# Optimization experiments

Measured on AMD Instinct MI355X. Metric: run time of the kernel, lower is better.

The kernel has to match this reference:

```python
import jax, jax.numpy as jnp
import numpy as np

N_EMBD = 1024
N_HEAD = 16

def setup_inputs() -> dict:
    key = jax.random.key(0)
    ks = jax.random.split(key, 5)
    s = 0.02
    x = jax.random.normal(ks[0], (4, 2048, N_EMBD), dtype=jnp.float32)
    W_attn = jax.random.normal(ks[1], (N_EMBD, 3 * N_EMBD), dtype=jnp.float32) * s
    b_attn = jnp.zeros((3 * N_EMBD,), dtype=jnp.float32)
    W_proj = jax.random.normal(ks[2], (N_EMBD, N_EMBD), dtype=jnp.float32) * s
    b_proj = jnp.zeros((N_EMBD,), dtype=jnp.float32)
    return {"x": x, "W_attn": W_attn, "b_attn": b_attn, "W_proj": W_proj, "b_proj": b_proj}

def reference(x, W_attn, b_attn, W_proj, b_proj):
    B, T, C = x.shape
    H = N_HEAD
    Dh = C // H
    qkv = x @ W_attn + b_attn                      # [B,T,3C]
    q, k, v = jnp.split(qkv, 3, axis=2)
    # [B,T,C] -> [B,H,T,Dh]
    q = q.reshape(B, T, H, Dh).transpose(0, 2, 1, 3)
    k = k.reshape(B, T, H, Dh).transpose(0, 2, 1, 3)
    v = v.reshape(B, T, H, Dh).transpose(0, 2, 1, 3)
    scale = 1.0 / jnp.sqrt(jnp.asarray(Dh, dtype=x.dtype))
    att = jnp.einsum('bhqd,bhkd->bhqk', q, k) * scale   # [B,H,T,T]
    causal = jnp.tril(jnp.ones((T, T), dtype=bool))
    att = jnp.where(causal[None, None], att, jnp.asarray(-jnp.inf, dtype=att.dtype))
    att = jax.nn.softmax(att, axis=-1)
    out = jnp.einsum('bhqk,bhkd->bhqd', att, v)          # [B,H,T,Dh]
    out = out.transpose(0, 2, 1, 3).reshape(B, T, C)
    return out @ W_proj + b_proj
```

## Files before the change

kernel.cpp:

```cpp
#include <hip/hip_runtime.h>
#include <hip/hip_bf16.h>
#include <cstdint>

typedef unsigned short u16;
typedef __attribute__((ext_vector_type(8))) short bf16x8;
typedef __attribute__((ext_vector_type(4))) float f32x4;

#define AS1 __attribute__((address_space(1)))
#define AS3 __attribute__((address_space(3)))

#define QSCALE_CONST 0.18033688011112042f
#define SMAX_CONST 8.0f

__device__ __forceinline__ u16 f2bf(float f) {
  union { float f; unsigned u; } v; v.f = f;
  unsigned u = v.u;
  return (u16)((u + 0x7fffu + ((u >> 16) & 1u)) >> 16);
}

__device__ __forceinline__ void gload_lds16(const void* g, const void* l) {
  __builtin_amdgcn_global_load_lds(
      (const AS1 unsigned int*)(uintptr_t)g,
      (AS3 unsigned int*)(unsigned int)(uintptr_t)l,
      16, 0, 0);
}

__global__ __launch_bounds__(256) void cast_bf16_kernel(
    const float* __restrict__ in, u16* __restrict__ out, int n) {
  int i = (blockIdx.x * 256 + threadIdx.x) * 4;
  if (i >= n) return;
  float4 f = *(const float4*)(in + i);
  ushort4 o;
  o.x = f2bf(f.x); o.y = f2bf(f.y); o.z = f2bf(f.z); o.w = f2bf(f.w);
  *(ushort4*)(out + i) = o;
}

__global__ __launch_bounds__(256) void transpose_cast_kernel(
    const float* __restrict__ in, u16* __restrict__ outT, int R, int C) {
  __shared__ float tile[32][33];
  const int c0 = blockIdx.x << 5, r0 = blockIdx.y << 5;
  const int x = threadIdx.x & 31, y = threadIdx.x >> 5;
#pragma unroll
  for (int yy = y; yy < 32; yy += 8)
    tile[yy][x] = in[(size_t)(r0 + yy) * C + c0 + x];
  __syncthreads();
#pragma unroll
  for (int yy = y; yy < 32; yy += 8)
    outT[(size_t)(c0 + yy) * R + r0 + x] = f2bf(tile[x][yy]);
}

template <typename OutT>
__global__ __launch_bounds__(256, 3) void gemm_bf16_kernel(
    const u16* __restrict__ A, const u16* __restrict__ Bt,
    const float* __restrict__ bias, OutT* __restrict__ Cmat,
    int M, int N, int K, int qcols) {
  __shared__ __attribute__((aligned(16))) u16 As[3][128 * 32];
  __shared__ __attribute__((aligned(16))) u16 Bs[3][128 * 32];

  const int nbn = N >> 7;
  const int nwg = (M >> 7) * nbn;
  int bid = blockIdx.x;
  if ((nwg & 7) == 0) {
    int cpx = nwg >> 3;
    bid = (bid & 7) * cpx + (bid >> 3);
  }
  const int bm = bid / nbn, bn = bid % nbn;

  const int tid = threadIdx.x;
  const int lane = tid & 63, wave = tid >> 6;
  const int g = lane >> 4, l15 = lane & 15;
  const int wrow = (wave >> 1) << 6, wcol = (wave & 1) << 6;

  const u16* Abase = A + (size_t)(bm << 7) * K;
  const u16* Bbase = Bt + (size_t)(bn << 7) * K;

  const int c0_ = wave * 64 + lane, c1_ = 256 + c0_;
  const int row0_ = c0_ >> 2, row1_ = c1_ >> 2;
  const size_t soff0 = (size_t)row0_ * K + ((c0_ & 3) ^ (row0_ & 3)) * 8;
  const size_t soff1 = (size_t)row1_ * K + ((c1_ & 3) ^ (row1_ & 3)) * 8;
  const int doff0 = c0_ * 8, doff1 = c1_ * 8;

  auto stage = [&](int buf, int k0) {
    gload_lds16(Abase + k0 + soff0, As[buf] + doff0);
    gload_lds16(Bbase + k0 + soff0, Bs[buf] + doff0);
    gload_lds16(Abase + k0 + soff1, As[buf] + doff1);
    gload_lds16(Bbase + k0 + soff1, Bs[buf] + doff1);
  };

  f32x4 zero = {0.f, 0.f, 0.f, 0.f};
  f32x4 acc[4][4];
#pragma unroll
  for (int i = 0; i < 4; ++i)
#pragma unroll
    for (int j = 0; j < 4; ++j) acc[i][j] = zero;

  const int NT = K >> 5;
  stage(0, 0);
  stage(1, 32);
#pragma unroll 1
  for (int kt = 0; kt < NT; ++kt) {
    const int cur = kt % 3;
    asm volatile("s_waitcnt lgkmcnt(0)" ::: "memory");
    __builtin_amdgcn_sched_barrier(0);
    if (kt < NT - 1) asm volatile("s_waitcnt vmcnt(4)" ::: "memory");
    else             asm volatile("s_waitcnt vmcnt(0)" ::: "memory");
    __builtin_amdgcn_s_barrier();
    if (kt + 2 < NT) stage((kt + 2) % 3, (kt + 2) << 5);

    const char* Ab = (const char*)As[cur];
    const char* Bb = (const char*)Bs[cur];
    bf16x8 af[4], bfr[4];
#pragma unroll
    for (int i = 0; i < 4; ++i) {
      int ra = wrow + i * 16 + l15;
      af[i] = *(const bf16x8*)(Ab + ra * 64 + ((g * 16) ^ ((ra & 3) << 4)));
      int rb = wcol + i * 16 + l15;
      bfr[i] = *(const bf16x8*)(Bb + rb * 64 + ((g * 16) ^ ((rb & 3) << 4)));
    }
#pragma unroll
    for (int i = 0; i < 4; ++i)
#pragma unroll
      for (int j = 0; j < 4; ++j)
        acc[i][j] = __builtin_amdgcn_mfma_f32_16x16x32_bf16(af[i], bfr[j], acc[i][j], 0, 0, 0);
  }

#pragma unroll
  for (int i = 0; i < 4; ++i) {
    int row0 = (bm << 7) + wrow + i * 16 + g * 4;
#pragma unroll
    for (int j = 0; j < 4; ++j) {
      int col = (bn << 7) + wcol + j * 16 + l15;
      float bv = bias[col];
      const bool qc = col < qcols;
#pragma unroll
      for (int r = 0; r < 4; ++r) {
        float v = acc[i][j][r] + bv;
        if (qc) v *= QSCALE_CONST;
        size_t idx = (size_t)(row0 + r) * N + col;
        if constexpr (sizeof(OutT) == 2)
          ((u16*)Cmat)[idx] = f2bf(v);
        else
          ((float*)Cmat)[idx] = v;
      }
    }
  }
}

__global__ __launch_bounds__(256, 2) void attn_kernel(
    const u16* __restrict__ qkv, u16* __restrict__ aout) {
  __shared__ __attribute__((aligned(16))) char KsB[2][8192];
  __shared__ __attribute__((aligned(16))) char VtB[2][8192];
  __shared__ __attribute__((aligned(16))) char PbB[4][4096];

  const int bh = blockIdx.x;
  const int b = bh >> 4, h = bh & 15;
  const int tid = threadIdx.x, lane = tid & 63, wave = tid >> 6;
  const int g = lane >> 4, l15 = lane & 15;

  const u16* qbase = qkv + (size_t)b * 2048 * 3072 + h * 64;
  const u16* kbase = qbase + 1024;
  const u16* vbase = qbase + 2048;

  const int krow0 = tid >> 3;
  const int ksc = (tid & 7) ^ (krow0 & 7);
  const size_t ksrc0 = (size_t)krow0 * 3072 + ksc * 8;
  const size_t ksrc1 = ksrc0 + (size_t)32 * 3072;
  const int vp_ = tid >> 3, vdh = tid & 7;
  const size_t vsrc = (size_t)(2 * vp_) * 3072 + vdh * 8;
  const int vkc = vp_ >> 2, vofs = (vp_ & 3) << 2;

  char* pb = PbB[wave];
  const f32x4 sinit = {-SMAX_CONST, -SMAX_CONST, -SMAX_CONST, -SMAX_CONST};
  f32x4 zero = {0.f, 0.f, 0.f, 0.f};

#pragma unroll 1
  for (int jj = 0; jj < 2; ++jj) {
    const int j = jj ? (15 - blockIdx.y) : blockIdx.y;
    const int q0 = j << 7;
    const int qrow = q0 + wave * 32;
    const int nt = 2 * j + 2;

    bf16x8 qfA[2], qfB[2];
#pragma unroll
    for (int kf = 0; kf < 2; ++kf) {
      qfA[kf] = *(const bf16x8*)(qbase + (size_t)(qrow + l15) * 3072 + kf * 32 + g * 8);
      qfB[kf] = *(const bf16x8*)(qbase + (size_t)(qrow + 16 + l15) * 3072 + kf * 32 + g * 8);
    }

    float lsumA = 0.f, lsumB = 0.f;
    f32x4 oA[4], oB[4];
#pragma unroll
    for (int d = 0; d < 4; ++d) { oA[d] = zero; oB[d] = zero; }

    gload_lds16(kbase + ksrc0, KsB[0] + wave * 1024);
    gload_lds16(kbase + ksrc1, KsB[0] + 4096 + wave * 1024);
    {
      bf16x8 v0 = *(const bf16x8*)(vbase + vsrc);
      bf16x8 v1 = *(const bf16x8*)(vbase + vsrc + 3072);
      char* vb = VtB[0];
#pragma unroll
      for (int q = 0; q < 8; ++q) {
        int d = vdh * 8 + q;
        int sig = q ^ vdh;
        unsigned pack = (unsigned)(u16)v0[q] | ((unsigned)(u16)v1[q] << 16);
        *(unsigned*)(vb + d * 128 + ((vkc ^ sig) << 4) + vofs) = pack;
      }
    }

    bf16x8 nv0, nv1;
#pragma unroll 1
    for (int t = 0; t < nt; ++t) {
      const int cur = t & 1;
      const int kv0 = t << 6;
      const bool pre = (t + 1 < nt);
      __syncthreads();

      if (pre) {
        const size_t nxt = (size_t)(t + 1) * 196608;
        gload_lds16(kbase + nxt + ksrc0, KsB[cur ^ 1] + wave * 1024);
        gload_lds16(kbase + nxt + ksrc1, KsB[cur ^ 1] + 4096 + wave * 1024);
        nv0 = *(const bf16x8*)(vbase + nxt + vsrc);
        nv1 = *(const bf16x8*)(vbase + nxt + vsrc + 3072);
      }

      if (qrow + 31 >= kv0) {
        const char* ks = KsB[cur];
        f32x4 sA[4], sB[4];
#pragma unroll
        for (int n = 0; n < 4; ++n) { sA[n] = sinit; sB[n] = sinit; }
#pragma unroll
        for (int kf = 0; kf < 2; ++kf)
#pragma unroll
          for (int n = 0; n < 4; ++n) {
            int row = n * 16 + l15;
            bf16x8 kfr = *(const bf16x8*)(ks + row * 128 + (((kf * 4 + g) ^ (row & 7)) << 4));
            sA[n] = __builtin_amdgcn_mfma_f32_16x16x32_bf16(kfr, qfA[kf], sA[n], 0, 0, 0);
            sB[n] = __builtin_amdgcn_mfma_f32_16x16x32_bf16(kfr, qfB[kf], sB[n], 0, 0, 0);
          }

        const int kvb = kv0 + g * 4;
        if (kv0 + 63 > qrow) {
          const int qgA = qrow + l15;
#pragma unroll
          for (int n = 0; n < 4; ++n)
#pragma unroll
            for (int r = 0; r < 4; ++r)
              if (kvb + n * 16 + r > qgA) sA[n][r] = -1e30f;
        }
        if (kv0 + 63 > qrow + 16) {
          const int qgB = qrow + 16 + l15;
#pragma unroll
          for (int n = 0; n < 4; ++n)
#pragma unroll
            for (int r = 0; r < 4; ++r)
              if (kvb + n * 16 + r > qgB) sB[n][r] = -1e30f;
        }

        float rsA = 0.f, rsB = 0.f;
#pragma unroll
        for (int n = 0; n < 4; ++n)
#pragma unroll
          for (int r = 0; r < 4; ++r) {
            float pA = __builtin_amdgcn_exp2f(sA[n][r]);
            float pB = __builtin_amdgcn_exp2f(sB[n][r]);
            sA[n][r] = pA; rsA += pA;
            sB[n][r] = pB; rsB += pB;
          }
        lsumA += rsA; lsumB += rsB;

#pragma unroll
        for (int n = 0; n < 4; ++n) {
          uint2 wA, wB;
          asm("v_cvt_pk_bf16_f32 %0, %1, %2" : "=v"(wA.x) : "v"(sA[n][0]), "v"(sA[n][1]));
          asm("v_cvt_pk_bf16_f32 %0, %1, %2" : "=v"(wA.y) : "v"(sA[n][2]), "v"(sA[n][3]));
          asm("v_cvt_pk_bf16_f32 %0, %1, %2" : "=v"(wB.x) : "v"(sB[n][0]), "v"(sB[n][1]));
          asm("v_cvt_pk_bf16_f32 %0, %1, %2" : "=v"(wB.y) : "v"(sB[n][2]), "v"(sB[n][3]));
          int c = n * 2 + (g >> 1);
          int boff = (((c ^ (l15 & 7)) << 4) | ((g & 1) << 3)) + l15 * 128;
          *(uint2*)(pb + boff) = wA;
          *(uint2*)(pb + 2048 + boff) = wB;
        }

        const char* vt = VtB[cur];
        bf16x8 pfA[2], pfB[2];
#pragma unroll
        for (int kf = 0; kf < 2; ++kf) {
          int poff = l15 * 128 + (((kf * 4 + g) ^ (l15 & 7)) << 4);
          pfA[kf] = *(const bf16x8*)(pb + poff);
          pfB[kf] = *(const bf16x8*)(pb + 2048 + poff);
        }
#pragma unroll
        for (int kf = 0; kf < 2; ++kf)
#pragma unroll
          for (int d = 0; d < 4; ++d) {
            int dr = d * 16 + l15;
            int sig = (dr & 7) ^ ((dr >> 3) & 7);
            bf16x8 vf = *(const bf16x8*)(vt + dr * 128 + (((kf * 4 + g) ^ sig) << 4));
            oA[d] = __builtin_amdgcn_mfma_f32_16x16x32_bf16(pfA[kf], vf, oA[d], 0, 0, 0);
            oB[d] = __builtin_amdgcn_mfma_f32_16x16x32_bf16(pfB[kf], vf, oB[d], 0, 0, 0);
          }
      }

      if (pre) {
        char* vb = VtB[cur ^ 1];
#pragma unroll
        for (int q = 0; q < 8; ++q) {
          int d = vdh * 8 + q;
          int sig = q ^ vdh;
          unsigned pack = (unsigned)(u16)nv0[q] | ((unsigned)(u16)nv1[q] << 16);
          *(unsigned*)(vb + d * 128 + ((vkc ^ sig) << 4) + vofs) = pack;
        }
      }
    }

    lsumA += __shfl_xor(lsumA, 16); lsumA += __shfl_xor(lsumA, 32);
    lsumB += __shfl_xor(lsumB, 16); lsumB += __shfl_xor(lsumB, 32);
    float invA[4], invB[4];
#pragma unroll
    for (int r = 0; r < 4; ++r) {
      invA[r] = __builtin_amdgcn_rcpf(__shfl(lsumA, g * 4 + r));
      invB[r] = __builtin_amdgcn_rcpf(__shfl(lsumB, g * 4 + r));
    }
    const size_t obase = (size_t)(b * 2048 + qrow) * 1024 + h * 64;
#pragma unroll
    for (int d = 0; d < 4; ++d)
#pragma unroll
      for (int r = 0; r < 4; ++r) {
        aout[obase + (size_t)(g * 4 + r) * 1024 + d * 16 + l15] = f2bf(oA[d][r] * invA[r]);
        aout[obase + (size_t)(16 + g * 4 + r) * 1024 + d * 16 + l15] = f2bf(oB[d][r] * invB[r]);
      }
  }
}

extern "C" void kernel_launch(void* const* d_in, const int* in_sizes, int n_in,
                              void* d_out, int out_size, void* d_ws, size_t ws_size,
                              hipStream_t stream) {
  const float* x      = (const float*)d_in[0];
  const float* W_attn = (const float*)d_in[1];
  const float* b_attn = (const float*)d_in[2];
  const float* W_proj = (const float*)d_in[3];
  const float* b_proj = (const float*)d_in[4];
  float* out = (float*)d_out;

  char* ws = (char*)d_ws;
  u16* xb   = (u16*)(ws);
  u16* Wat  = (u16*)(ws + (size_t)16 * 1024 * 1024);
  u16* Wpt  = (u16*)(ws + (size_t)22 * 1024 * 1024);
  u16* qkv  = (u16*)(ws + (size_t)24 * 1024 * 1024);
  u16* aout = (u16*)(ws + (size_t)72 * 1024 * 1024);

  cast_bf16_kernel<<<8192, 256, 0, stream>>>(x, xb, 8388608);
  transpose_cast_kernel<<<dim3(96, 32), 256, 0, stream>>>(W_attn, Wat, 1024, 3072);
  transpose_cast_kernel<<<dim3(32, 32), 256, 0, stream>>>(W_proj, Wpt, 1024, 1024);
  gemm_bf16_kernel<u16><<<1536, 256, 0, stream>>>(xb, Wat, b_attn, qkv, 8192, 3072, 1024, 1024);
  attn_kernel<<<dim3(64, 8), 256, 0, stream>>>(qkv, aout);
  gemm_bf16_kernel<float><<<512, 256, 0, stream>>>(aout, Wpt, b_proj, out, 8192, 1024, 1024, 0);
}
```

Measured before the change: 166.7 us.

## Use 256x256-tile 8-wave GEMM kernel for QKV projection

Adds a new bf16 GEMM kernel with 256x256 output tiles, 512 threads (8 waves, each computing 128x64), triple-buffered LDS staging and a split two-phase MFMA schedule that interleaves the A and B loads with compute. It replaces the 128x128 GEMM for the QKV projection, cutting the launch to 384 workgroups. Larger tiles raise arithmetic intensity and reduce global/L2 traffic per FLOP. In exchange, register pressure and LDS use per workgroup go up, and fewer workgroups means worse load balance across the CUs.

```diff
diff --git a/kernel.cpp b/kernel.cpp
--- a/kernel.cpp
+++ b/kernel.cpp
@@ -47,6 +47,131 @@
 #pragma unroll
   for (int yy = y; yy < 32; yy += 8)
     outT[(size_t)(c0 + yy) * R + r0 + x] = f2bf(tile[x][yy]);
+}
+
+__global__ __launch_bounds__(512, 2) void gemm256_kernel(
+    const u16* __restrict__ A, const u16* __restrict__ Bt,
+    const float* __restrict__ bias, u16* __restrict__ Cmat,
+    int M, int N, int K, int qcols) {
+  __shared__ __attribute__((aligned(16))) u16 As[3][256 * 32];
+  __shared__ __attribute__((aligned(16))) u16 Bs[3][256 * 32];
+
+  const int nbn = N >> 8;
+  const int nwg = (M >> 8) * nbn;
+  int bid = blockIdx.x;
+  if ((nwg & 7) == 0) {
+    int cpx = nwg >> 3;
+    bid = (bid & 7) * cpx + (bid >> 3);
+  }
+  const int bm = bid / nbn, bn = bid % nbn;
+
+  const int tid = threadIdx.x;
+  const int lane = tid & 63, wave = tid >> 6;
+  const int g = lane >> 4, l15 = lane & 15;
+  const int wm = wave >> 2, wn = wave & 3;
+
+  const u16* Abase = A + (size_t)(bm << 8) * K;
+  const u16* Bbase = Bt + (size_t)(bn << 8) * K;
+
+  const int c0_ = tid, c1_ = 512 + tid;
+  const int r0_ = c0_ >> 2, r1_ = c1_ >> 2;
+  const size_t soff0 = (size_t)r0_ * K + ((c0_ & 3) ^ (r0_ & 3)) * 8;
+  const size_t soff1 = (size_t)r1_ * K + ((c1_ & 3) ^ (r1_ & 3)) * 8;
+  const int doff0 = c0_ * 8, doff1 = c1_ * 8;
+
+  auto stageA = [&](int buf, int k0) {
+    gload_lds16(Abase + k0 + soff0, As[buf] + doff0);
+    gload_lds16(Abase + k0 + soff1, As[buf] + doff1);
+  };
+  auto stageB = [&](int buf, int k0) {
+    gload_lds16(Bbase + k0 + soff0, Bs[buf] + doff0);
+    gload_lds16(Bbase + k0 + soff1, Bs[buf] + doff1);
+  };
+
+  f32x4 zero = {0.f, 0.f, 0.f, 0.f};
+  f32x4 acc[8][4];
+#pragma unroll
+  for (int i = 0; i < 8; ++i)
+#pragma unroll
+    for (int j = 0; j < 4; ++j) acc[i][j] = zero;
+
+  const int NT = K >> 5;
+  stageA(0, 0); stageB(0, 0);
+  stageA(1, 32); stageB(1, 32);
+  asm volatile("s_waitcnt vmcnt(4)" ::: "memory");
+  __builtin_amdgcn_s_barrier();
+  __builtin_amdgcn_sched_barrier(0);
+
+#pragma unroll 1
+  for (int kt = 0; kt < NT; ++kt) {
+    const int cur = kt % 3, nxt = (kt + 2) % 3;
+    const char* Ab = (const char*)As[cur];
+    const char* Bb = (const char*)Bs[cur];
+
+    bf16x8 af[4], bfr[4];
+#pragma unroll
+    for (int i = 0; i < 4; ++i) {
+      int ra = wm * 128 + i * 16 + l15;
+      af[i] = *(const bf16x8*)(Ab + ra * 64 + ((g ^ (ra & 3)) << 4));
+    }
+#pragma unroll
+    for (int j = 0; j < 4; ++j) {
+      int rb = wn * 64 + j * 16 + l15;
+      bfr[j] = *(const bf16x8*)(Bb + rb * 64 + ((g ^ (rb & 3)) << 4));
+    }
+    if (kt + 2 < NT) stageA(nxt, (kt + 2) << 5);
+    __builtin_amdgcn_s_barrier();
+    asm volatile("s_waitcnt lgkmcnt(0)" ::: "memory");
+    __builtin_amdgcn_sched_barrier(0);
+    __builtin_amdgcn_s_setprio(1);
+#pragma unroll
+    for (int i = 0; i < 4; ++i)
+#pragma unroll
+      for (int j = 0; j < 4; ++j)
+        acc[i][j] = __builtin_amdgcn_mfma_f32_16x16x32_bf16(af[i], bfr[j], acc[i][j], 0, 0, 0);
+    __builtin_amdgcn_s_setprio(0);
+    __builtin_amdgcn_s_barrier();
+    __builtin_amdgcn_sched_barrier(0);
+
+    bf16x8 ag[4];
+#pragma unroll
+    for (int i = 0; i < 4; ++i) {
+      int ra = wm * 128 + (i + 4) * 16 + l15;
+      ag[i] = *(const bf16x8*)(Ab + ra * 64 + ((g ^ (ra & 3)) << 4));
+    }
+    if (kt + 2 < NT) stageB(nxt, (kt + 2) << 5);
+    __builtin_amdgcn_s_barrier();
+    asm volatile("s_waitcnt lgkmcnt(0)" ::: "memory");
+    __builtin_amdgcn_sched_barrier(0);
+    __builtin_amdgcn_s_setprio(1);
+#pragma unroll
+    for (int i = 0; i < 4; ++i)
+#pragma unroll
+      for (int j = 0; j < 4; ++j)
+        acc[i + 4][j] = __builtin_amdgcn_mfma_f32_16x16x32_bf16(ag[i], bfr[j], acc[i + 4][j], 0, 0, 0);
+    __builtin_amdgcn_s_setprio(0);
+    if (kt < NT - 2)       asm volatile("s_waitcnt vmcnt(4)" ::: "memory");
+    else if (kt == NT - 2) asm volatile("s_waitcnt vmcnt(0)" ::: "memory");
+    __builtin_amdgcn_s_barrier();
+    __builtin_amdgcn_sched_barrier(0);
+  }
+
+#pragma unroll
+  for (int i = 0; i < 8; ++i) {
+    int row0 = (bm << 8) + wm * 128 + i * 16 + g * 4;
+#pragma unroll
+    for (int j = 0; j < 4; ++j) {
+      int col = (bn << 8) + wn * 64 + j * 16 + l15;
+      float bv = bias[col];
+      const bool qc = col < qcols;
+#pragma unroll
+      for (int r = 0; r < 4; ++r) {
+        float v = acc[i][j][r] + bv;
+        if (qc) v *= QSCALE_CONST;
+        Cmat[(size_t)(row0 + r) * N + col] = f2bf(v);
+      }
+    }
+  }
 }
 
 template <typename OutT>
@@ -352,7 +477,7 @@
   cast_bf16_kernel<<<8192, 256, 0, stream>>>(x, xb, 8388608);
   transpose_cast_kernel<<<dim3(96, 32), 256, 0, stream>>>(W_attn, Wat, 1024, 3072);
   transpose_cast_kernel<<<dim3(32, 32), 256, 0, stream>>>(W_proj, Wpt, 1024, 1024);
-  gemm_bf16_kernel<u16><<<1536, 256, 0, stream>>>(xb, Wat, b_attn, qkv, 8192, 3072, 1024, 1024);
+  gemm256_kernel<<<384, 512, 0, stream>>>(xb, Wat, b_attn, qkv, 8192, 3072, 1024, 1024);
   attn_kernel<<<dim3(64, 8), 256, 0, stream>>>(qkv, aout);
   gemm_bf16_kernel<float><<<512, 256, 0, stream>>>(aout, Wpt, b_proj, out, 8192, 1024, 1024, 0);
 }
```

After: 170.5 us. 1.02x slower.

## Enlarge GEMM tiles to 128x256 with 8 waves and double-buffered 64-wide K stages

Applied to the files above, without the earlier changes.

Rewrites the bf16 GEMM to use 512-thread workgroups computing 128x256 output tiles, with K stepped in 64-wide chunks split into two 32-wide LDS sub-stages that are double-buffered. The next tile's global-to-LDS loads are issued between the fragment reads and the MFMAs, and the MFMA block is wrapped in s_setprio, to overlap memory with compute and improve operand reuse per LDS load. The LDS swizzle changes to an (row>>1)-based XOR. This trades more LDS per workgroup and fewer resident workgroups, plus fewer blocks for the second GEMM (256), for larger tiles and fewer barriers per K.

```diff
diff --git a/kernel.cpp b/kernel.cpp
--- a/kernel.cpp
+++ b/kernel.cpp
@@ -50,14 +50,14 @@
 }
 
 template <typename OutT>
-__global__ __launch_bounds__(256, 3) void gemm_bf16_kernel(
+__global__ __launch_bounds__(512, 2) void gemm1_kernel(
     const u16* __restrict__ A, const u16* __restrict__ Bt,
     const float* __restrict__ bias, OutT* __restrict__ Cmat,
     int M, int N, int K, int qcols) {
-  __shared__ __attribute__((aligned(16))) u16 As[3][128 * 32];
-  __shared__ __attribute__((aligned(16))) u16 Bs[3][128 * 32];
-
-  const int nbn = N >> 7;
+  __shared__ __attribute__((aligned(16))) u16 LA[2][2][128 * 32];
+  __shared__ __attribute__((aligned(16))) u16 LB[2][2][256 * 32];
+
+  const int nbn = N >> 8;
   const int nwg = (M >> 7) * nbn;
   int bid = blockIdx.x;
   if ((nwg & 7) == 0) {
@@ -69,22 +69,23 @@
   const int tid = threadIdx.x;
   const int lane = tid & 63, wave = tid >> 6;
   const int g = lane >> 4, l15 = lane & 15;
-  const int wrow = (wave >> 1) << 6, wcol = (wave & 1) << 6;
+  const int wm = wave >> 2, wn = wave & 3;
 
   const u16* Abase = A + (size_t)(bm << 7) * K;
-  const u16* Bbase = Bt + (size_t)(bn << 7) * K;
-
-  const int c0_ = wave * 64 + lane, c1_ = 256 + c0_;
-  const int row0_ = c0_ >> 2, row1_ = c1_ >> 2;
-  const size_t soff0 = (size_t)row0_ * K + ((c0_ & 3) ^ (row0_ & 3)) * 8;
-  const size_t soff1 = (size_t)row1_ * K + ((c1_ & 3) ^ (row1_ & 3)) * 8;
-  const int doff0 = c0_ * 8, doff1 = c1_ * 8;
-
-  auto stage = [&](int buf, int k0) {
-    gload_lds16(Abase + k0 + soff0, As[buf] + doff0);
-    gload_lds16(Bbase + k0 + soff0, Bs[buf] + doff0);
-    gload_lds16(Abase + k0 + soff1, As[buf] + doff1);
-    gload_lds16(Bbase + k0 + soff1, Bs[buf] + doff1);
+  const u16* Bbase = Bt + (size_t)(bn << 8) * K;
+
+  const int rA = tid >> 2;
+  const size_t aoff = (size_t)rA * K + (((tid & 3) ^ ((rA >> 1) & 3)) * 8);
+  const int rB0 = tid >> 2;
+  const size_t boff0 = (size_t)rB0 * K + (((tid & 3) ^ ((rB0 >> 1) & 3)) * 8);
+  const int cB1 = 512 + tid, rB1 = cB1 >> 2;
+  const size_t boff1 = (size_t)rB1 * K + (((cB1 & 3) ^ ((rB1 >> 1) & 3)) * 8);
+
+  auto stageG = [&](int buf, int s, int kt) {
+    const size_t kof = (size_t)kt * 64 + s * 32;
+    gload_lds16(Abase + kof + aoff, &LA[buf][s][0] + tid * 8);
+    gload_lds16(Bbase + kof + boff0, &LB[buf][s][0] + tid * 8);
+    gload_lds16(Bbase + kof + boff1, &LB[buf][s][0] + (512 + tid) * 8);
   };
 
   f32x4 zero = {0.f, 0.f, 0.f, 0.f};
@@ -94,42 +95,56 @@
 #pragma unroll
     for (int j = 0; j < 4; ++j) acc[i][j] = zero;
 
-  const int NT = K >> 5;
-  stage(0, 0);
-  stage(1, 32);
+  const int NT = K >> 6;
+
+  stageG(0, 0, 0);
+  stageG(0, 1, 0);
+  asm volatile("s_waitcnt vmcnt(3)" ::: "memory");
+  __builtin_amdgcn_s_barrier();
+  __builtin_amdgcn_sched_barrier(0);
+
 #pragma unroll 1
   for (int kt = 0; kt < NT; ++kt) {
-    const int cur = kt % 3;
-    asm volatile("s_waitcnt lgkmcnt(0)" ::: "memory");
-    __builtin_amdgcn_sched_barrier(0);
-    if (kt < NT - 1) asm volatile("s_waitcnt vmcnt(4)" ::: "memory");
-    else             asm volatile("s_waitcnt vmcnt(0)" ::: "memory");
-    __builtin_amdgcn_s_barrier();
-    if (kt + 2 < NT) stage((kt + 2) % 3, (kt + 2) << 5);
-
-    const char* Ab = (const char*)As[cur];
-    const char* Bb = (const char*)Bs[cur];
-    bf16x8 af[4], bfr[4];
-#pragma unroll
-    for (int i = 0; i < 4; ++i) {
-      int ra = wrow + i * 16 + l15;
-      af[i] = *(const bf16x8*)(Ab + ra * 64 + ((g * 16) ^ ((ra & 3) << 4)));
-      int rb = wcol + i * 16 + l15;
-      bfr[i] = *(const bf16x8*)(Bb + rb * 64 + ((g * 16) ^ ((rb & 3) << 4)));
-    }
-#pragma unroll
-    for (int i = 0; i < 4; ++i)
-#pragma unroll
-      for (int j = 0; j < 4; ++j)
-        acc[i][j] = __builtin_amdgcn_mfma_f32_16x16x32_bf16(af[i], bfr[j], acc[i][j], 0, 0, 0);
+    const int cbuf = kt & 1, nbuf = cbuf ^ 1;
+    const bool more = (kt + 1 < NT);
+#pragma unroll
+    for (int s = 0; s < 2; ++s) {
+      const char* Ab = (const char*)&LA[cbuf][s][0];
+      const char* Bb = (const char*)&LB[cbuf][s][0];
+      bf16x8 af[4], bfr[4];
+#pragma unroll
+      for (int i = 0; i < 4; ++i) {
+        int ra = wm * 64 + i * 16 + l15;
+        af[i] = *(const bf16x8*)(Ab + ra * 64 + ((g ^ ((ra >> 1) & 3)) << 4));
+      }
+#pragma unroll
+      for (int j = 0; j < 4; ++j) {
+        int rb = wn * 64 + j * 16 + l15;
+        bfr[j] = *(const bf16x8*)(Bb + rb * 64 + ((g ^ ((rb >> 1) & 3)) << 4));
+      }
+      if (more) stageG(nbuf, s, kt + 1);
+      asm volatile("s_waitcnt lgkmcnt(0)" ::: "memory");
+      __builtin_amdgcn_sched_barrier(0);
+      __builtin_amdgcn_s_setprio(1);
+#pragma unroll
+      for (int i = 0; i < 4; ++i)
+#pragma unroll
+        for (int j = 0; j < 4; ++j)
+          acc[i][j] = __builtin_amdgcn_mfma_f32_16x16x32_bf16(af[i], bfr[j], acc[i][j], 0, 0, 0);
+      __builtin_amdgcn_s_setprio(0);
+      if (more)            asm volatile("s_waitcnt vmcnt(3)" ::: "memory");
+      else if (s == 0)     asm volatile("s_waitcnt vmcnt(0)" ::: "memory");
+      __builtin_amdgcn_s_barrier();
+      __builtin_amdgcn_sched_barrier(0);
+    }
   }
 
 #pragma unroll
   for (int i = 0; i < 4; ++i) {
-    int row0 = (bm << 7) + wrow + i * 16 + g * 4;
+    int row0 = (bm << 7) + wm * 64 + i * 16 + g * 4;
 #pragma unroll
     for (int j = 0; j < 4; ++j) {
-      int col = (bn << 7) + wcol + j * 16 + l15;
+      int col = (bn << 8) + wn * 64 + j * 16 + l15;
       float bv = bias[col];
       const bool qc = col < qcols;
 #pragma unroll
@@ -352,7 +367,7 @@
   cast_bf16_kernel<<<8192, 256, 0, stream>>>(x, xb, 8388608);
   transpose_cast_kernel<<<dim3(96, 32), 256, 0, stream>>>(W_attn, Wat, 1024, 3072);
   transpose_cast_kernel<<<dim3(32, 32), 256, 0, stream>>>(W_proj, Wpt, 1024, 1024);
-  gemm_bf16_kernel<u16><<<1536, 256, 0, stream>>>(xb, Wat, b_attn, qkv, 8192, 3072, 1024, 1024);
+  gemm1_kernel<u16><<<768, 512, 0, stream>>>(xb, Wat, b_attn, qkv, 8192, 3072, 1024, 1024);
   attn_kernel<<<dim3(64, 8), 256, 0, stream>>>(qkv, aout);
-  gemm_bf16_kernel<float><<<512, 256, 0, stream>>>(aout, Wpt, b_proj, out, 8192, 1024, 1024, 0);
-}
+  gemm1_kernel<float><<<256, 512, 0, stream>>>(aout, Wpt, b_proj, out, 8192, 1024, 1024, 0);
+}
```

New measurement: 172.6 us. 1.04x slower.
